# Kernel optimization log

Measured on AMD Instinct MI355X. Metric: run time of the kernel, lower is better.

## Reference

```python
import jax, jax.numpy as jnp
import numpy as np

N_NODES = 100_000
N_EDGES = 3_200_000
F_IN = 64
HID = 16
N_CLASSES = 4


def setup_inputs() -> dict:
    key = jax.random.key(0)
    ks = jax.random.split(key, 9)
    x = jax.random.normal(ks[0], (N_NODES, F_IN), dtype=jnp.float32)
    edge_index = jax.random.randint(ks[1], (2, N_EDGES), 0, N_NODES, dtype=jnp.int64)
    edge_weight = jax.random.uniform(ks[2], (N_EDGES,), dtype=jnp.float32)
    # Glorot-style init for the three GCN layer weights, zero bias (PyG default)
    W1 = jax.random.normal(ks[3], (F_IN, HID), dtype=jnp.float32) * (1.0 / np.sqrt(F_IN))
    b1 = jnp.zeros((HID,), jnp.float32)
    W3 = jax.random.normal(ks[4], (HID, HID), dtype=jnp.float32) * (1.0 / np.sqrt(HID))
    b3 = jnp.zeros((HID,), jnp.float32)
    W2 = jax.random.normal(ks[5], (HID, N_CLASSES), dtype=jnp.float32) * (1.0 / np.sqrt(HID))
    b2 = jnp.zeros((N_CLASSES,), jnp.float32)
    return {"x": x, "edge_index": edge_index, "edge_weight": edge_weight,
            "W1": W1, "b1": b1, "W3": W3, "b3": b3, "W2": W2, "b2": b2}


def reference(x, edge_index, edge_weight, W1, b1, W3, b3, W2, b2):
    n = x.shape[0]
    # GCNConv default: add self-loops with weight 1, symmetric deg^-1/2 norm
    loop = jnp.arange(n, dtype=edge_index.dtype)
    row = jnp.concatenate([edge_index[0], loop])  # source nodes
    col = jnp.concatenate([edge_index[1], loop])  # target nodes
    ew = jnp.concatenate([edge_weight, jnp.ones((n,), edge_weight.dtype)])
    deg = jax.ops.segment_sum(ew, col, num_segments=n)
    dinv = jnp.where(deg > 0, jax.lax.rsqrt(deg), 0.0)
    norm = dinv[row] * ew * dinv[col]  # [E+N]

    def gcn_conv(h, W, b):
        h = h @ W                                  # [N, out] small matmul first
        msg = norm[:, None] * h[row]               # gather + scale, [E+N, out]
        return jax.ops.segment_sum(msg, col, num_segments=n) + b

    h = jax.nn.relu(gcn_conv(x, W1, b1))
    # dropout is identity in eval mode (training=False)
    h = jax.nn.relu(gcn_conv(h, W3, b3))
    h = gcn_conv(h, W2, b2)
    return jax.nn.log_softmax(h, axis=1)
```

## Files before the change

### kernel.cpp

```cpp
#include <hip/hip_runtime.h>
#include <math.h>

#define NN 100000
#define NE 3200000
#define F_IN 64
#define HID 16
#define NC 4

#define SZB 512
#define NB 196
#define CAP 17920
#define CH 8192
#define NCH 391

typedef _Float16 half_t;
typedef _Float16 h4f __attribute__((ext_vector_type(4)));

__global__ __launch_bounds__(256) void k_initcur(int* __restrict__ cursor) {
    int i = threadIdx.x;
    if (i < NB) cursor[i] = i * CAP;
}

__global__ __launch_bounds__(1024) void k_bin(const int* __restrict__ row,
                                              const int* __restrict__ col,
                                              const float* __restrict__ ew,
                                              int* __restrict__ cursor,
                                              uint2* __restrict__ bin) {
    __shared__ int h[NB];
    __shared__ int lstart[NB + 1];
    __shared__ int gbase[NB];
    __shared__ int ps[256];
    __shared__ uint2 stage[CH];
    int tid = threadIdx.x;
    for (int i = tid; i < NB; i += 1024) h[i] = 0;
    __syncthreads();
    int e0 = blockIdx.x * CH;
    int e1 = min(e0 + CH, NE);
    int eCnt = e1 - e0;
    for (int i = e0 + tid * 4; i < e1; i += 1024 * 4) {
        int4 c4 = *(const int4*)(col + i);
        atomicAdd(&h[c4.x >> 9], 1);
        atomicAdd(&h[c4.y >> 9], 1);
        atomicAdd(&h[c4.z >> 9], 1);
        atomicAdd(&h[c4.w >> 9], 1);
    }
    __syncthreads();
    int c0 = (tid < NB) ? h[tid] : 0;
    if (tid < 256) ps[tid] = c0;
    for (int off = 1; off < 256; off <<= 1) {
        __syncthreads();
        int v = (tid < 256 && tid >= off) ? ps[tid - off] : 0;
        __syncthreads();
        if (tid < 256) ps[tid] += v;
    }
    __syncthreads();
    if (tid < NB) {
        int ex = ps[tid] - c0;
        lstart[tid] = ex;
        h[tid] = ex;
        if (c0) gbase[tid] = atomicAdd(&cursor[tid], c0);
    }
    if (tid == 0) lstart[NB] = eCnt;
    __syncthreads();
    for (int i = e0 + tid * 4; i < e1; i += 1024 * 4) {
        int4 c4 = *(const int4*)(col + i);
        int4 r4 = *(const int4*)(row + i);
        float4 w4 = *(const float4*)(ew + i);
        int p;
        p = atomicAdd(&h[c4.x >> 9], 1);
        stage[p] = make_uint2(((unsigned)r4.x << 9) | (c4.x & 511), __float_as_uint(w4.x));
        p = atomicAdd(&h[c4.y >> 9], 1);
        stage[p] = make_uint2(((unsigned)r4.y << 9) | (c4.y & 511), __float_as_uint(w4.y));
        p = atomicAdd(&h[c4.z >> 9], 1);
        stage[p] = make_uint2(((unsigned)r4.z << 9) | (c4.z & 511), __float_as_uint(w4.z));
        p = atomicAdd(&h[c4.w >> 9], 1);
        stage[p] = make_uint2(((unsigned)r4.w << 9) | (c4.w & 511), __float_as_uint(w4.w));
    }
    __syncthreads();
    for (int i = tid; i < eCnt; i += 1024) {
        int lo = 0, hi = NB;
        while (hi - lo > 1) {
            int mid = (lo + hi) >> 1;
            if (lstart[mid] <= i) lo = mid; else hi = mid;
        }
        bin[gbase[lo] + (i - lstart[lo])] = stage[i];
    }
}

__global__ __launch_bounds__(1024) void k_sort(const uint2* __restrict__ bin,
                                               const int* __restrict__ cursor,
                                               unsigned* __restrict__ ekey,
                                               half_t* __restrict__ ew16,
                                               int2* __restrict__ nodeptr2,
                                               float* __restrict__ dinv) {
    __shared__ int cnt[SZB];
    __shared__ float wdeg[SZB];
    __shared__ int ps[SZB];
    __shared__ int curp[SZB];
    __shared__ unsigned skey_st[CAP];
    __shared__ half_t sw_st[CAP];
    int b = blockIdx.x, tid = threadIdx.x;
    if (tid < SZB) { cnt[tid] = 0; wdeg[tid] = 0.0f; }
    __syncthreads();
    int s = b * CAP, e = cursor[b];
    int m = e - s;
    for (int i = s + tid; i < e; i += 1024) {
        uint2 u = bin[i];
        int cl = u.x & 511;
        atomicAdd(&cnt[cl], 1);
        atomicAdd(&wdeg[cl], __uint_as_float(u.y));
    }
    __syncthreads();
    if (tid < SZB) ps[tid] = cnt[tid];
    for (int off = 1; off < SZB; off <<= 1) {
        __syncthreads();
        int v = (tid < SZB && tid >= off) ? ps[tid - off] : 0;
        __syncthreads();
        if (tid < SZB) ps[tid] += v;
    }
    __syncthreads();
    if (tid < SZB) {
        int ex = ps[tid] - cnt[tid];
        curp[tid] = ex;
        int n = b * SZB + tid;
        if (n < NN) {
            nodeptr2[n] = make_int2(s + ex, s + ex + cnt[tid]);
            dinv[n] = rsqrtf(1.0f + wdeg[tid]);
        }
    }
    __syncthreads();
    for (int i = s + tid; i < e; i += 1024) {
        uint2 u = bin[i];
        int cl = u.x & 511;
        int pos = atomicAdd(&curp[cl], 1);
        skey_st[pos] = u.x >> 9;
        sw_st[pos] = (half_t)__uint_as_float(u.y);
    }
    __syncthreads();
    for (int i = tid; i < m; i += 1024) {
        ekey[s + i] = skey_st[i];
        ew16[s + i] = sw_st[i];
    }
}

__global__ __launch_bounds__(256) void k_xform1(const float* __restrict__ x,
                                                const float* __restrict__ W,
                                                const float* __restrict__ dinv,
                                                half_t* __restrict__ tt) {
    __shared__ float Ws[F_IN * HID];
    for (int i = threadIdx.x; i < F_IN * HID; i += 256) Ws[i] = W[i];
    __syncthreads();
    int n = blockIdx.x * blockDim.x + threadIdx.x;
    if (n >= NN) return;
    float acc[HID];
#pragma unroll
    for (int j = 0; j < HID; j++) acc[j] = 0.0f;
    const float4* xp = (const float4*)(x + (size_t)n * F_IN);
#pragma unroll
    for (int k4 = 0; k4 < F_IN / 4; k4++) {
        float4 v = xp[k4];
        int k = k4 * 4;
#pragma unroll
        for (int j = 0; j < HID; j++) {
            acc[j] += v.x * Ws[(k + 0) * HID + j];
            acc[j] += v.y * Ws[(k + 1) * HID + j];
            acc[j] += v.z * Ws[(k + 2) * HID + j];
            acc[j] += v.w * Ws[(k + 3) * HID + j];
        }
    }
    float di = dinv[n];
    h4f* op = (h4f*)(tt + (size_t)n * HID);
#pragma unroll
    for (int g = 0; g < 4; g++) {
        h4f o;
        o.x = (half_t)(di * acc[g * 4 + 0]);
        o.y = (half_t)(di * acc[g * 4 + 1]);
        o.z = (half_t)(di * acc[g * 4 + 2]);
        o.w = (half_t)(di * acc[g * 4 + 3]);
        op[g] = o;
    }
}

template <int DN>
__global__ __launch_bounds__(256) void k_aggf(const unsigned* __restrict__ ekey,
                                              const half_t* __restrict__ ew16,
                                              const int2* __restrict__ nptr,
                                              const half_t* __restrict__ tt_in,
                                              const float* __restrict__ bias,
                                              const float* __restrict__ dinv,
                                              const float* __restrict__ Wn,
                                              half_t* __restrict__ tt_out) {
    __shared__ float Ws[HID * DN];
    if (threadIdx.x < HID * DN) Ws[threadIdx.x] = Wn[threadIdx.x];
    __syncthreads();
    int tid = blockIdx.x * 256 + threadIdx.x;
    int n = tid >> 2;
    int l = tid & 3;
    if (n >= NN) return;
    int2 p = nptr[n];
    const h4f* ttp = (const h4f*)tt_in;
    h4f sv = ttp[n * 4 + l];
    float ax = 0.f, ay = 0.f, az = 0.f, aw = 0.f;
    int abase = p.x & ~3;
    for (int base = abase; base < p.y; base += 4) {
        int4 k4 = *(const int4*)(ekey + base);
        h4f w4 = *(const h4f*)(ew16 + base);
        bool ok0 = (base + 0 >= p.x) & (base + 0 < p.y);
        bool ok1 = (base + 1 >= p.x) & (base + 1 < p.y);
        bool ok2 = (base + 2 >= p.x) & (base + 2 < p.y);
        bool ok3 = (base + 3 >= p.x) & (base + 3 < p.y);
        float w0 = ok0 ? (float)w4.x : 0.f; int r0 = ok0 ? k4.x : 0;
        float w1 = ok1 ? (float)w4.y : 0.f; int r1 = ok1 ? k4.y : 0;
        float w2 = ok2 ? (float)w4.z : 0.f; int r2 = ok2 ? k4.z : 0;
        float w3 = ok3 ? (float)w4.w : 0.f; int r3 = ok3 ? k4.w : 0;
        h4f v0 = ttp[r0 * 4 + l];
        h4f v1 = ttp[r1 * 4 + l];
        h4f v2 = ttp[r2 * 4 + l];
        h4f v3 = ttp[r3 * 4 + l];
        ax += w0 * (float)v0.x; ay += w0 * (float)v0.y; az += w0 * (float)v0.z; aw += w0 * (float)v0.w;
        ax += w1 * (float)v1.x; ay += w1 * (float)v1.y; az += w1 * (float)v1.z; aw += w1 * (float)v1.w;
        ax += w2 * (float)v2.x; ay += w2 * (float)v2.y; az += w2 * (float)v2.z; aw += w2 * (float)v2.w;
        ax += w3 * (float)v3.x; ay += w3 * (float)v3.y; az += w3 * (float)v3.z; aw += w3 * (float)v3.w;
    }
    float di = dinv[n];
    const float4* b4p = (const float4*)bias;
    float4 b4 = b4p[l];
    float hreg[4];
    hreg[0] = fmaxf(b4.x + di * (ax + (float)sv.x), 0.f);
    hreg[1] = fmaxf(b4.y + di * (ay + (float)sv.y), 0.f);
    hreg[2] = fmaxf(b4.z + di * (az + (float)sv.z), 0.f);
    hreg[3] = fmaxf(b4.w + di * (aw + (float)sv.w), 0.f);
    if (DN == 16) {
        float ox = 0.f, oy = 0.f, oz = 0.f, ow = 0.f;
#pragma unroll
        for (int k = 0; k < HID; k++) {
            float hk = __shfl(hreg[k & 3], k >> 2, 4);
            const float4 wk = *(const float4*)&Ws[k * 16 + 4 * l];
            ox += hk * wk.x; oy += hk * wk.y; oz += hk * wk.z; ow += hk * wk.w;
        }
        h4f ov;
        ov.x = (half_t)(di * ox); ov.y = (half_t)(di * oy);
        ov.z = (half_t)(di * oz); ov.w = (half_t)(di * ow);
        ((h4f*)tt_out)[n * 4 + l] = ov;
    } else {
        float o = 0.f;
#pragma unroll
        for (int k = 0; k < HID; k++) {
            float hk = __shfl(hreg[k & 3], k >> 2, 4);
            o += hk * Ws[k * DN + l];
        }
        tt_out[(size_t)n * DN + l] = (half_t)(di * o);
    }
}

__global__ __launch_bounds__(256) void k_agg4sm(const unsigned* __restrict__ ekey,
                                                const half_t* __restrict__ ew16,
                                                const int2* __restrict__ nptr,
                                                const half_t* __restrict__ tt,
                                                const float* __restrict__ bias,
                                                const float* __restrict__ dinv,
                                                float* __restrict__ out) {
    int tid = blockIdx.x * 256 + threadIdx.x;
    int n = tid >> 2;
    int l = tid & 3;
    if (n >= NN) return;
    int2 p = nptr[n];
    float self = (float)tt[n * 4 + l];
    float acc = 0.f;
    int abase = p.x & ~3;
    for (int base = abase; base < p.y; base += 4) {
        int4 k4 = *(const int4*)(ekey + base);
        h4f w4 = *(const h4f*)(ew16 + base);
        bool ok0 = (base + 0 >= p.x) & (base + 0 < p.y);
        bool ok1 = (base + 1 >= p.x) & (base + 1 < p.y);
        bool ok2 = (base + 2 >= p.x) & (base + 2 < p.y);
        bool ok3 = (base + 3 >= p.x) & (base + 3 < p.y);
        float w0 = ok0 ? (float)w4.x : 0.f; int r0 = ok0 ? k4.x : 0;
        float w1 = ok1 ? (float)w4.y : 0.f; int r1 = ok1 ? k4.y : 0;
        float w2 = ok2 ? (float)w4.z : 0.f; int r2 = ok2 ? k4.z : 0;
        float w3 = ok3 ? (float)w4.w : 0.f; int r3 = ok3 ? k4.w : 0;
        acc += w0 * (float)tt[r0 * 4 + l];
        acc += w1 * (float)tt[r1 * 4 + l];
        acc += w2 * (float)tt[r2 * 4 + l];
        acc += w3 * (float)tt[r3 * 4 + l];
    }
    float di = dinv[n];
    float logit = bias[l] + di * (acc + self);
    float m = logit;
    m = fmaxf(m, __shfl_xor(m, 1, 4));
    m = fmaxf(m, __shfl_xor(m, 2, 4));
    float ex = expf(logit - m);
    float s = ex;
    s += __shfl_xor(s, 1, 4);
    s += __shfl_xor(s, 2, 4);
    out[n * 4 + l] = logit - m - logf(s);
}

extern "C" void kernel_launch(void* const* d_in, const int* in_sizes, int n_in,
                              void* d_out, int out_size, void* d_ws, size_t ws_size,
                              hipStream_t stream) {
    const float* x  = (const float*)d_in[0];
    const int*   ei = (const int*)d_in[1];
    const float* ew = (const float*)d_in[2];
    const float* W1 = (const float*)d_in[3];
    const float* b1 = (const float*)d_in[4];
    const float* W3 = (const float*)d_in[5];
    const float* b3 = (const float*)d_in[6];
    const float* W2 = (const float*)d_in[7];
    const float* b2 = (const float*)d_in[8];
    float* out = (float*)d_out;

    const int* row = ei;
    const int* col = ei + NE;

    const size_t NEP = (size_t)NB * CAP;
    char* ws = (char*)d_ws;
    size_t off = 0;
    float*    dinv     = (float*)(ws + off);    off += 400000;
    int2*     nodeptr2 = (int2*)(ws + off);     off += 800000;
    int*      cursor   = (int*)(ws + off);      off += 1024;
    unsigned* ekey     = (unsigned*)(ws + off); off += NEP * 4;
    half_t*   ew16     = (half_t*)(ws + off);   off += NEP * 2;
    uint2*    bin      = (uint2*)(ws + off);    off += NEP * 8;
    half_t*   tt1      = (half_t*)(ws + off);   off += (size_t)NN * HID * 2;
    half_t*   tt2      = (half_t*)(ws + off);   off += (size_t)NN * HID * 2;
    half_t*   tt3      = (half_t*)(ws + off);   off += (size_t)NN * NC * 2;

    k_initcur<<<1, 256, 0, stream>>>(cursor);
    k_bin<<<NCH, 1024, 0, stream>>>(row, col, ew, cursor, bin);
    k_sort<<<NB, 1024, 0, stream>>>(bin, cursor, ekey, ew16, nodeptr2, dinv);

    int gN = (NN + 255) / 256;
    int gA = (NN * 4 + 255) / 256;

    k_xform1<<<gN, 256, 0, stream>>>(x, W1, dinv, tt1);
    k_aggf<HID><<<gA, 256, 0, stream>>>(ekey, ew16, nodeptr2, tt1, b1, dinv, W3, tt2);
    k_aggf<NC><<<gA, 256, 0, stream>>>(ekey, ew16, nodeptr2, tt2, b3, dinv, W2, tt3);
    k_agg4sm<<<gA, 256, 0, stream>>>(ekey, ew16, nodeptr2, tt3, b2, dinv, out);
}
```

Baseline: 255.1 us.

## Halve bucket size and pad per-node edge lists to multiples of four

The counting sort now uses 256-node buckets (391 blocks), so k_sort gets more parallelism and a smaller shared footprint. Each node's edge segment is padded to a multiple of four with zero-key, zero-weight entries. This lets the aggregation loops drop the per-lane bounds checks and start on aligned boundaries. In exchange the padding adds extra gathers of node 0, and writes that would overflow a bucket's capacity are silently dropped, which is only safe when bucket occupancy stays under the cap.

```diff
diff --git a/kernel.cpp b/kernel.cpp
--- a/kernel.cpp
+++ b/kernel.cpp
@@ -7,16 +7,16 @@
 #define HID 16
 #define NC 4
 
-#define SZB 512
-#define NB 196
-#define CAP 17920
+#define SZB 256
+#define NB 391
+#define CAP 10240
 #define CH 8192
 #define NCH 391
 
 typedef _Float16 half_t;
 typedef _Float16 h4f __attribute__((ext_vector_type(4)));
 
-__global__ __launch_bounds__(256) void k_initcur(int* __restrict__ cursor) {
+__global__ __launch_bounds__(512) void k_initcur(int* __restrict__ cursor) {
     int i = threadIdx.x;
     if (i < NB) cursor[i] = i * CAP;
 }
@@ -29,7 +29,7 @@
     __shared__ int h[NB];
     __shared__ int lstart[NB + 1];
     __shared__ int gbase[NB];
-    __shared__ int ps[256];
+    __shared__ int ps[512];
     __shared__ uint2 stage[CH];
     int tid = threadIdx.x;
     for (int i = tid; i < NB; i += 1024) h[i] = 0;
@@ -39,19 +39,19 @@
     int eCnt = e1 - e0;
     for (int i = e0 + tid * 4; i < e1; i += 1024 * 4) {
         int4 c4 = *(const int4*)(col + i);
-        atomicAdd(&h[c4.x >> 9], 1);
-        atomicAdd(&h[c4.y >> 9], 1);
-        atomicAdd(&h[c4.z >> 9], 1);
-        atomicAdd(&h[c4.w >> 9], 1);
+        atomicAdd(&h[c4.x >> 8], 1);
+        atomicAdd(&h[c4.y >> 8], 1);
+        atomicAdd(&h[c4.z >> 8], 1);
+        atomicAdd(&h[c4.w >> 8], 1);
     }
     __syncthreads();
     int c0 = (tid < NB) ? h[tid] : 0;
-    if (tid < 256) ps[tid] = c0;
-    for (int off = 1; off < 256; off <<= 1) {
+    if (tid < 512) ps[tid] = c0;
+    for (int off = 1; off < 512; off <<= 1) {
         __syncthreads();
-        int v = (tid < 256 && tid >= off) ? ps[tid - off] : 0;
+        int v = (tid < 512 && tid >= off) ? ps[tid - off] : 0;
         __syncthreads();
-        if (tid < 256) ps[tid] += v;
+        if (tid < 512) ps[tid] += v;
     }
     __syncthreads();
     if (tid < NB) {
@@ -67,14 +67,14 @@
         int4 r4 = *(const int4*)(row + i);
         float4 w4 = *(const float4*)(ew + i);
         int p;
-        p = atomicAdd(&h[c4.x >> 9], 1);
-        stage[p] = make_uint2(((unsigned)r4.x << 9) | (c4.x & 511), __float_as_uint(w4.x));
-        p = atomicAdd(&h[c4.y >> 9], 1);
-        stage[p] = make_uint2(((unsigned)r4.y << 9) | (c4.y & 511), __float_as_uint(w4.y));
-        p = atomicAdd(&h[c4.z >> 9], 1);
-        stage[p] = make_uint2(((unsigned)r4.z << 9) | (c4.z & 511), __float_as_uint(w4.z));
-        p = atomicAdd(&h[c4.w >> 9], 1);
-        stage[p] = make_uint2(((unsigned)r4.w << 9) | (c4.w & 511), __float_as_uint(w4.w));
+        p = atomicAdd(&h[c4.x >> 8], 1);
+        stage[p] = make_uint2(((unsigned)r4.x << 8) | (c4.x & 255), __float_as_uint(w4.x));
+        p = atomicAdd(&h[c4.y >> 8], 1);
+        stage[p] = make_uint2(((unsigned)r4.y << 8) | (c4.y & 255), __float_as_uint(w4.y));
+        p = atomicAdd(&h[c4.z >> 8], 1);
+        stage[p] = make_uint2(((unsigned)r4.z << 8) | (c4.z & 255), __float_as_uint(w4.z));
+        p = atomicAdd(&h[c4.w >> 8], 1);
+        stage[p] = make_uint2(((unsigned)r4.w << 8) | (c4.w & 255), __float_as_uint(w4.w));
     }
     __syncthreads();
     for (int i = tid; i < eCnt; i += 1024) {
@@ -83,7 +83,9 @@
             int mid = (lo + hi) >> 1;
             if (lstart[mid] <= i) lo = mid; else hi = mid;
         }
-        bin[gbase[lo] + (i - lstart[lo])] = stage[i];
+        int d = gbase[lo] + (i - lstart[lo]);
+        if (d < (lo + 1) * CAP)
+            bin[d] = stage[i];
     }
 }
 
@@ -97,21 +99,23 @@
     __shared__ float wdeg[SZB];
     __shared__ int ps[SZB];
     __shared__ int curp[SZB];
+    __shared__ int mpad_s;
     __shared__ unsigned skey_st[CAP];
     __shared__ half_t sw_st[CAP];
     int b = blockIdx.x, tid = threadIdx.x;
     if (tid < SZB) { cnt[tid] = 0; wdeg[tid] = 0.0f; }
     __syncthreads();
-    int s = b * CAP, e = cursor[b];
-    int m = e - s;
+    int s = b * CAP;
+    int e = min(cursor[b], s + CAP);
     for (int i = s + tid; i < e; i += 1024) {
         uint2 u = bin[i];
-        int cl = u.x & 511;
+        int cl = u.x & 255;
         atomicAdd(&cnt[cl], 1);
         atomicAdd(&wdeg[cl], __uint_as_float(u.y));
     }
     __syncthreads();
-    if (tid < SZB) ps[tid] = cnt[tid];
+    int pc = (tid < SZB) ? ((cnt[tid] + 3) & ~3) : 0;
+    if (tid < SZB) ps[tid] = pc;
     for (int off = 1; off < SZB; off <<= 1) {
         __syncthreads();
         int v = (tid < SZB && tid >= off) ? ps[tid - off] : 0;
@@ -120,24 +124,31 @@
     }
     __syncthreads();
     if (tid < SZB) {
-        int ex = ps[tid] - cnt[tid];
+        int ex = ps[tid] - pc;
         curp[tid] = ex;
         int n = b * SZB + tid;
         if (n < NN) {
-            nodeptr2[n] = make_int2(s + ex, s + ex + cnt[tid]);
+            nodeptr2[n] = make_int2(s + ex, s + ex + pc);
             dinv[n] = rsqrtf(1.0f + wdeg[tid]);
         }
+        if (tid == SZB - 1) mpad_s = ps[tid];
+    }
+    __syncthreads();
+    int mpad = mpad_s;
+    for (int i = tid; i < mpad; i += 1024) {
+        skey_st[i] = 0u;
+        sw_st[i] = (half_t)0.0f;
     }
     __syncthreads();
     for (int i = s + tid; i < e; i += 1024) {
         uint2 u = bin[i];
-        int cl = u.x & 511;
+        int cl = u.x & 255;
         int pos = atomicAdd(&curp[cl], 1);
-        skey_st[pos] = u.x >> 9;
+        skey_st[pos] = u.x >> 8;
         sw_st[pos] = (half_t)__uint_as_float(u.y);
     }
     __syncthreads();
-    for (int i = tid; i < m; i += 1024) {
+    for (int i = tid; i < mpad; i += 1024) {
         ekey[s + i] = skey_st[i];
         ew16[s + i] = sw_st[i];
     }
@@ -201,22 +212,14 @@
     const h4f* ttp = (const h4f*)tt_in;
     h4f sv = ttp[n * 4 + l];
     float ax = 0.f, ay = 0.f, az = 0.f, aw = 0.f;
-    int abase = p.x & ~3;
-    for (int base = abase; base < p.y; base += 4) {
+    for (int base = p.x; base < p.y; base += 4) {
         int4 k4 = *(const int4*)(ekey + base);
         h4f w4 = *(const h4f*)(ew16 + base);
-        bool ok0 = (base + 0 >= p.x) & (base + 0 < p.y);
-        bool ok1 = (base + 1 >= p.x) & (base + 1 < p.y);
-        bool ok2 = (base + 2 >= p.x) & (base + 2 < p.y);
-        bool ok3 = (base + 3 >= p.x) & (base + 3 < p.y);
-        float w0 = ok0 ? (float)w4.x : 0.f; int r0 = ok0 ? k4.x : 0;
-        float w1 = ok1 ? (float)w4.y : 0.f; int r1 = ok1 ? k4.y : 0;
-        float w2 = ok2 ? (float)w4.z : 0.f; int r2 = ok2 ? k4.z : 0;
-        float w3 = ok3 ? (float)w4.w : 0.f; int r3 = ok3 ? k4.w : 0;
-        h4f v0 = ttp[r0 * 4 + l];
-        h4f v1 = ttp[r1 * 4 + l];
-        h4f v2 = ttp[r2 * 4 + l];
-        h4f v3 = ttp[r3 * 4 + l];
+        h4f v0 = ttp[k4.x * 4 + l];
+        h4f v1 = ttp[k4.y * 4 + l];
+        h4f v2 = ttp[k4.z * 4 + l];
+        h4f v3 = ttp[k4.w * 4 + l];
+        float w0 = (float)w4.x, w1 = (float)w4.y, w2 = (float)w4.z, w3 = (float)w4.w;
         ax += w0 * (float)v0.x; ay += w0 * (float)v0.y; az += w0 * (float)v0.z; aw += w0 * (float)v0.w;
         ax += w1 * (float)v1.x; ay += w1 * (float)v1.y; az += w1 * (float)v1.z; aw += w1 * (float)v1.w;
         ax += w2 * (float)v2.x; ay += w2 * (float)v2.y; az += w2 * (float)v2.z; aw += w2 * (float)v2.w;
@@ -267,22 +270,13 @@
     int2 p = nptr[n];
     float self = (float)tt[n * 4 + l];
     float acc = 0.f;
-    int abase = p.x & ~3;
-    for (int base = abase; base < p.y; base += 4) {
+    for (int base = p.x; base < p.y; base += 4) {
         int4 k4 = *(const int4*)(ekey + base);
         h4f w4 = *(const h4f*)(ew16 + base);
-        bool ok0 = (base + 0 >= p.x) & (base + 0 < p.y);
-        bool ok1 = (base + 1 >= p.x) & (base + 1 < p.y);
-        bool ok2 = (base + 2 >= p.x) & (base + 2 < p.y);
-        bool ok3 = (base + 3 >= p.x) & (base + 3 < p.y);
-        float w0 = ok0 ? (float)w4.x : 0.f; int r0 = ok0 ? k4.x : 0;
-        float w1 = ok1 ? (float)w4.y : 0.f; int r1 = ok1 ? k4.y : 0;
-        float w2 = ok2 ? (float)w4.z : 0.f; int r2 = ok2 ? k4.z : 0;
-        float w3 = ok3 ? (float)w4.w : 0.f; int r3 = ok3 ? k4.w : 0;
-        acc += w0 * (float)tt[r0 * 4 + l];
-        acc += w1 * (float)tt[r1 * 4 + l];
-        acc += w2 * (float)tt[r2 * 4 + l];
-        acc += w3 * (float)tt[r3 * 4 + l];
+        acc += (float)w4.x * (float)tt[k4.x * 4 + l];
+        acc += (float)w4.y * (float)tt[k4.y * 4 + l];
+        acc += (float)w4.z * (float)tt[k4.z * 4 + l];
+        acc += (float)w4.w * (float)tt[k4.w * 4 + l];
     }
     float di = dinv[n];
     float logit = bias[l] + di * (acc + self);
@@ -318,7 +312,7 @@
     size_t off = 0;
     float*    dinv     = (float*)(ws + off);    off += 400000;
     int2*     nodeptr2 = (int2*)(ws + off);     off += 800000;
-    int*      cursor   = (int*)(ws + off);      off += 1024;
+    int*      cursor   = (int*)(ws + off);      off += 2048;
     unsigned* ekey     = (unsigned*)(ws + off); off += NEP * 4;
     half_t*   ew16     = (half_t*)(ws + off);   off += NEP * 2;
     uint2*    bin      = (uint2*)(ws + off);    off += NEP * 8;
@@ -326,7 +320,7 @@
     half_t*   tt2      = (half_t*)(ws + off);   off += (size_t)NN * HID * 2;
     half_t*   tt3      = (half_t*)(ws + off);   off += (size_t)NN * NC * 2;
 
-    k_initcur<<<1, 256, 0, stream>>>(cursor);
+    k_initcur<<<1, 512, 0, stream>>>(cursor);
     k_bin<<<NCH, 1024, 0, stream>>>(row, col, ew, cursor, bin);
     k_sort<<<NB, 1024, 0, stream>>>(bin, cursor, ekey, ew16, nodeptr2, dinv);
 
```

Result: no change. 255.1 us (+0.0%).
